# Kernel optimization log

Hardware: AMD Instinct MI355X
Metric: run time of the kernel (lower is better)

The kernel has to match this reference:

```python
import jax, jax.numpy as jnp
import numpy as np

N_USERS, N_NEWS, N_ENT, N_REL, D, K, NNZ = 10000, 10000, 100000, 32, 64, 20, 500000

def setup_inputs() -> dict:
    key = jax.random.key(0)
    ks = jax.random.split(key, 10)
    return {
        "user_emb": jax.random.normal(ks[0], (N_USERS, D), jnp.float32),
        "news_embeding": jax.random.normal(ks[1], (N_NEWS, D), jnp.float32),
        "entity_emb": jax.random.normal(ks[2], (N_ENT, D), jnp.float32),
        "relation_emb": jax.random.normal(ks[3], (N_REL, D), jnp.float32),
        "news_entities": jax.random.randint(ks[4], (N_NEWS, K), 0, N_ENT),
        "news_relations": jnp.zeros((N_NEWS, K), jnp.int32),  # code forces relation id 0 for news
        "neigh_entities": jax.random.randint(ks[5], (N_ENT, K), 0, N_ENT),
        "neigh_relations": jax.random.randint(ks[6], (N_ENT, K), 0, N_REL),
        "interact_rows": jax.random.randint(ks[7], (NNZ,), 0, N_USERS),
        "interact_cols": jax.random.randint(ks[8], (NNZ,), 0, N_NEWS),
        "interact_vals": jax.random.uniform(ks[9], (NNZ,), jnp.float32),
    }

def _sim_hrt(head, tail, rel):
    # head: [N,D], tail/rel: [N,K,D]
    tail_rel = tail * rel                              # [N,K,D]
    head_rel = head[:, None, :] * rel                  # [N,K,D]
    # NOTE: original norms over the NEIGHBOR dim (dim=1), yielding [N,1,D]
    hnorm = jnp.sqrt(jnp.sum(head_rel * head_rel, axis=1))  # [N,D]
    att = jnp.einsum('nkd,nd->nk', tail_rel, hnorm)    # [N,K]
    return att * att

def _agg(head_emb, neigh_ent_emb, neigh_rel_emb):
    w = jax.nn.softmax(_sim_hrt(head_emb, neigh_ent_emb, neigh_rel_emb), axis=-1)
    return jnp.einsum('nk,nkd->nd', w, neigh_ent_emb)

def reference(user_emb, news_embeding, entity_emb, relation_emb,
              news_entities, news_relations, neigh_entities, neigh_relations,
              interact_rows, interact_cols, interact_vals):
    # news aggregation (newsid = arange -> identity gather on news_embeding)
    news_ne = entity_emb[news_entities]                # [N_news,K,D]
    news_nr = relation_emb[news_relations]             # [N_news,K,D]
    news_agg = _agg(news_embeding, news_ne, news_nr)   # [N_news,D]
    # entity aggregation (entities = arange -> identity gather on entity_emb)
    ent_ne = entity_emb[neigh_entities]                # [N_ent,K,D]
    ent_nr = relation_emb[neigh_relations]             # [N_ent,K,D]
    entity_agg = _agg(entity_emb, ent_ne, ent_nr)      # [N_ent,D]
    # user aggregation: sparse interact_mat @ news_agg via segment_sum
    gathered = interact_vals[:, None] * news_agg[interact_cols]  # [NNZ,D]
    user_agg = jax.ops.segment_sum(gathered, interact_rows, num_segments=N_USERS)
    score = jax.nn.softmax(user_emb @ news_agg.T, axis=-1)       # [N_users,N_news]
    user_agg = user_agg + (score @ news_agg) * user_agg
    return (news_agg, entity_agg, user_agg)
```

## Files before the change

### kernel.cpp

```cpp
#include <hip/hip_runtime.h>
#include <hip/hip_bf16.h>


#define DD 64
#define KK 20
#define NCHUNK 313
#define NSL 20
#define NSTRIP 157
#define NUPAD 10048
#define ATSTRIDE 10016
#define PST32 20

#define ATTN_BLOCKS 785
#define AGG_ENT_BLOCKS 12500

typedef __attribute__((ext_vector_type(8))) short short8;
typedef __attribute__((ext_vector_type(4))) float f32x4;

__device__ __forceinline__ unsigned short f2bf(float x) {
    union { __hip_bfloat16 h; unsigned short u; } cv;
    cv.h = __float2bfloat16(x);
    return cv.u;
}
__device__ __forceinline__ float bfu2f(unsigned short u) {
    return __uint_as_float(((unsigned)u) << 16);
}
#define MFMA16(a, b, c) __builtin_amdgcn_mfma_f32_16x16x32_bf16((a), (b), (c), 0, 0, 0)

__device__ __forceinline__
void agg_body(const float* __restrict__ head_emb, const float* __restrict__ ent_emb,
              const float* __restrict__ rel_emb,
              const int* __restrict__ ent_idx, const int* __restrict__ rel_idx,
              float* __restrict__ outp, int bid)
{
    int w = threadIdx.x >> 6;
    int lane = threadIdx.x & 63;
    int half = lane >> 5;
    int l = lane & 31;
    int n0 = bid * 8 + w * 2;

    float2 head = *(const float2*)(head_emb + (long)(n0 + half) * DD + 2 * l);

    float2 tail[KK], trp[KK];
    float2 s2 = make_float2(0.f, 0.f);
#pragma unroll
    for (int k = 0; k < KK; ++k) {
        int ei0 = ent_idx[n0 * KK + k];
        int ei1 = ent_idx[(n0 + 1) * KK + k];
        int ri0 = rel_idx[n0 * KK + k];
        int ri1 = rel_idx[(n0 + 1) * KK + k];
        int e = half ? ei1 : ei0;
        int r = half ? ri1 : ri0;
        float2 rv = *(const float2*)(rel_emb + (long)r * DD + 2 * l);
        float2 tv = *(const float2*)(ent_emb + (long)e * DD + 2 * l);
        tail[k] = tv;
        trp[k] = make_float2(tv.x * rv.x, tv.y * rv.y);
        s2.x = fmaf(rv.x, rv.x, s2.x);
        s2.y = fmaf(rv.y, rv.y, s2.y);
    }
    float2 hn;
    hn.x = fabsf(head.x) * sqrtf(s2.x);
    hn.y = fabsf(head.y) * sqrtf(s2.y);

    float att[KK];
#pragma unroll
    for (int k = 0; k < KK; ++k) {
        float v = fmaf(trp[k].y, hn.y, trp[k].x * hn.x);
#pragma unroll
        for (int m = 1; m < 32; m <<= 1)
            v += __shfl_xor(v, m, 64);
        att[k] = v * v;
    }
    float mx = att[0];
#pragma unroll
    for (int k = 1; k < KK; ++k) mx = fmaxf(mx, att[k]);
    float den = 0.f;
#pragma unroll
    for (int k = 0; k < KK; ++k) { att[k] = __expf(att[k] - mx); den += att[k]; }
    float inv = 1.f / den;
    float2 o = make_float2(0.f, 0.f);
#pragma unroll
    for (int k = 0; k < KK; ++k) {
        o.x = fmaf(att[k], tail[k].x, o.x);
        o.y = fmaf(att[k], tail[k].y, o.y);
    }
    o.x *= inv; o.y *= inv;
    *(float2*)(outp + (long)(n0 + half) * DD + 2 * l) = o;
}

__global__ __launch_bounds__(256)
void agg_kernel(const float* __restrict__ head_emb, const float* __restrict__ ent_emb,
                const float* __restrict__ rel_emb,
                const int* __restrict__ ent_idx, const int* __restrict__ rel_idx,
                float* __restrict__ outp, int N)
{
    int n0 = blockIdx.x * 8 + (threadIdx.x >> 6) * 2;
    if (n0 >= N) return;
    agg_body(head_emb, ent_emb, rel_emb, ent_idx, rel_idx, outp, blockIdx.x);
}

__global__ __launch_bounds__(256)
void cvt_kernel(const float* __restrict__ src, unsigned short* __restrict__ dst,
                int n_src, int n_total)
{
    int t = blockIdx.x * 256 + threadIdx.x;
    if (t >= n_total) return;
    float v = (t < n_src) ? src[t] : 0.f;
    dst[t] = f2bf(v);
}

__global__ __launch_bounds__(256)
void transpose_kernel(const float* __restrict__ src, unsigned short* __restrict__ AT)
{
    __shared__ float T[128][65];
    int t = threadIdx.x;
    int nb = blockIdx.x * 128;
    const float4* s4 = (const float4*)src;
#pragma unroll
    for (int i = 0; i < 8; ++i) {
        int f = i * 256 + t;
        int row = f >> 4;
        int c4 = f & 15;
        int gr = nb + row;
        float4 v = make_float4(0.f, 0.f, 0.f, 0.f);
        if (gr < 10000) v = s4[(long)gr * 16 + c4];
        T[row][c4 * 4 + 0] = v.x;
        T[row][c4 * 4 + 1] = v.y;
        T[row][c4 * 4 + 2] = v.z;
        T[row][c4 * 4 + 3] = v.w;
    }
    __syncthreads();
    int d = t >> 2;
    int seg = t & 3;
#pragma unroll
    for (int g = 0; g < 8; ++g) {
        int nl = seg * 32 + g * 4;
        int n = nb + nl;
        if (n + 3 < ATSTRIDE) {
            int base = seg * 32;
            ushort4 oh;
            oh.x = f2bf(T[base + 2 * g][d]);
            oh.y = f2bf(T[base + 16 + 2 * g][d]);
            oh.z = f2bf(T[base + 2 * g + 1][d]);
            oh.w = f2bf(T[base + 16 + 2 * g + 1][d]);
            *(ushort4*)(AT + (long)d * ATSTRIDE + n) = oh;
        }
    }
}

__global__ __launch_bounds__(256)
void hist_kernel(const int* __restrict__ rows, int* __restrict__ cnt, int nnz)
{
    int e = blockIdx.x * 256 + threadIdx.x;
    if (e < nnz) atomicAdd(&cnt[rows[e]], 1);
}

__global__ __launch_bounds__(256)
void scan_kernel(const int* __restrict__ cnt, int* __restrict__ offs, int* __restrict__ cur)
{
    __shared__ int ssum[256];
    int t = threadIdx.x;
    int loc[40];
    int s = 0;
#pragma unroll
    for (int i = 0; i < 40; ++i) { loc[i] = s; s += cnt[t * 40 + i]; }
    ssum[t] = s;
    __syncthreads();
    int val = s;
    for (int off = 1; off < 256; off <<= 1) {
        int v = (t >= off) ? ssum[t - off] : 0;
        __syncthreads();
        val += v;
        ssum[t] = val;
        __syncthreads();
    }
    int excl = val - s;
#pragma unroll
    for (int i = 0; i < 40; ++i) {
        int o = excl + loc[i];
        offs[t * 40 + i] = o;
        cur[t * 40 + i] = o;
    }
}

__global__ __launch_bounds__(256)
void fill_kernel(const int* __restrict__ rows, int* __restrict__ cur,
                 int* __restrict__ eid, int nnz)
{
    int e = blockIdx.x * 256 + threadIdx.x;
    if (e < nnz) {
        int p = atomicAdd(&cur[rows[e]], 1);
        eid[p] = e;
    }
}

__global__ __launch_bounds__(256)
void gather_kernel(const int* __restrict__ offs, const int* __restrict__ eid,
                   const int* __restrict__ cols, const float* __restrict__ vals,
                   const float* __restrict__ A, float* __restrict__ seg, int n_users)
{
    int w = threadIdx.x >> 6;
    int lane = threadIdx.x & 63;
    int u = blockIdx.x * 4 + w;
    if (u >= n_users) return;
    int s0 = offs[u], s1 = offs[u + 1];
    float acc = 0.f;
    for (int i = s0; i < s1; ++i) {
        int e = eid[i];
        float v = vals[e];
        int c = cols[e];
        acc = fmaf(v, A[(long)c * DD + lane], acc);
    }
    seg[(long)u * DD + lane] = acc;
}

__device__ __forceinline__
void attn_body(const unsigned short* __restrict__ Ubf,
               const unsigned short* __restrict__ Bbf,
               const unsigned short* __restrict__ ATbf,
               float* __restrict__ num, float* __restrict__ den,
               unsigned int* __restrict__ PuAll, int bid)
{
    int w = threadIdx.x >> 6;
    int lane = threadIdx.x & 63;
    int quad = lane >> 4;
    int l15 = lane & 15;
    int wid = bid * 4 + w;
    int strip = wid % NSTRIP;
    int slice = wid / NSTRIP;
    int user0 = strip * 64;

    short8 ua0[4], ua1[4];
#pragma unroll
    for (int t = 0; t < 4; ++t) {
        const short* up = (const short*)Ubf + ((long)(user0 + t * 16 + l15)) * 64;
        ua0[t] = *(const short8*)(up + quad * 8);
        ua1[t] = *(const short8*)(up + 32 + quad * 8);
    }

    f32x4 numC[4][4];
    float dena[4][4];
#pragma unroll
    for (int t = 0; t < 4; ++t)
#pragma unroll
        for (int c = 0; c < 4; ++c) {
            numC[t][c] = (f32x4){0.f, 0.f, 0.f, 0.f};
            dena[t][c] = 0.f;
        }

    for (int ch = slice; ch < NCHUNK; ch += NSL) {
        int nb = ch * 32;
        const short* bh = (const short*)Bbf + ((long)(nb + l15)) * 64;
        short8 b00 = *(const short8*)(bh + quad * 8);
        short8 b01 = *(const short8*)(bh + 32 + quad * 8);
        short8 b10 = *(const short8*)(bh + 16 * 64 + quad * 8);
        short8 b11 = *(const short8*)(bh + 16 * 64 + 32 + quad * 8);

        short8 vh[4];
#pragma unroll
        for (int c = 0; c < 4; ++c)
            vh[c] = *(const short8*)((const short*)ATbf +
                    ((long)(16 * c + l15)) * ATSTRIDE + nb + quad * 8);

        bool vlo = (nb + l15) < 10000;
        bool vhi = (nb + 16 + l15) < 10000;
        f32x4 z = {0.f, 0.f, 0.f, 0.f};
#pragma unroll
        for (int p = 0; p < 2; ++p) {
#pragma unroll
            for (int tt = 0; tt < 2; ++tt) {
                int t = p * 2 + tt;
                f32x4 Llo = MFMA16(ua0[t], b00, z);
                Llo = MFMA16(ua1[t], b01, Llo);
                f32x4 Lhi = MFMA16(ua0[t], b10, z);
                Lhi = MFMA16(ua1[t], b11, Lhi);
                unsigned int* Pt = PuAll + (w * 2 + tt) * (16 * PST32);
#pragma unroll
                for (int r = 0; r < 4; ++r) {
                    float plo = vlo ? __expf(fminf(Llo[r], 70.f)) : 0.f;
                    float phi = vhi ? __expf(fminf(Lhi[r], 70.f)) : 0.f;
                    __hip_bfloat162 pk2 = __float22bfloat162_rn(make_float2(plo, phi));
                    unsigned int pk;
                    __builtin_memcpy(&pk, &pk2, 4);
                    Pt[(quad * 4 + r) * PST32 + l15] = pk;
                    dena[t][r] += __uint_as_float(pk << 16)
                                + __uint_as_float(pk & 0xffff0000u);
                }
            }
            short8 ap[2];
#pragma unroll
            for (int tt = 0; tt < 2; ++tt)
                ap[tt] = *(const short8*)((const short*)(PuAll + (w * 2 + tt) * (16 * PST32)) +
                         l15 * (PST32 * 2) + quad * 8);
#pragma unroll
            for (int c = 0; c < 4; ++c)
#pragma unroll
                for (int tt = 0; tt < 2; ++tt)
                    numC[p * 2 + tt][c] = MFMA16(ap[tt], vh[c], numC[p * 2 + tt][c]);
        }
    }

#pragma unroll
    for (int t = 0; t < 4; ++t)
#pragma unroll
        for (int r = 0; r < 4; ++r) {
#pragma unroll
            for (int m = 1; m < 16; m <<= 1)
                dena[t][r] += __shfl_xor(dena[t][r], m, 64);
        }
    if (l15 == 0) {
#pragma unroll
        for (int t = 0; t < 4; ++t)
#pragma unroll
            for (int r = 0; r < 4; ++r)
                atomicAdd(&den[user0 + t * 16 + quad * 4 + r], dena[t][r]);
    }
#pragma unroll
    for (int t = 0; t < 4; ++t)
#pragma unroll
        for (int c = 0; c < 4; ++c)
#pragma unroll
            for (int r = 0; r < 4; ++r)
                atomicAdd(&num[(long)(user0 + t * 16 + quad * 4 + r) * DD + c * 16 + l15],
                          numC[t][c][r]);
}

__global__ __launch_bounds__(256)
void attn_kernel(const unsigned short* __restrict__ Ubf,
                 const unsigned short* __restrict__ Bbf,
                 const unsigned short* __restrict__ ATbf,
                 float* __restrict__ num, float* __restrict__ den)
{
    __shared__ __align__(16) unsigned int Pu[8][16 * PST32];
    if (blockIdx.x * 4 + (threadIdx.x >> 6) >= NSTRIP * NSL) return;
    attn_body(Ubf, Bbf, ATbf, num, den, &Pu[0][0], blockIdx.x);
}

__global__ __launch_bounds__(256)
void fused_kernel(const unsigned short* __restrict__ Ubf,
                  const unsigned short* __restrict__ Bbf,
                  const unsigned short* __restrict__ ATbf,
                  float* __restrict__ num, float* __restrict__ den,
                  const float* __restrict__ ent_emb, const float* __restrict__ rel_emb,
                  const int* __restrict__ ent_idx, const int* __restrict__ rel_idx,
                  float* __restrict__ out_ent)
{
    __shared__ __align__(16) unsigned int Pu[8][16 * PST32];
    if (blockIdx.x < ATTN_BLOCKS) {
        attn_body(Ubf, Bbf, ATbf, num, den, &Pu[0][0], blockIdx.x);
    } else {
        agg_body(ent_emb, ent_emb, rel_emb, ent_idx, rel_idx, out_ent,
                 blockIdx.x - ATTN_BLOCKS);
    }
}

__global__ __launch_bounds__(256)
void final_kernel(const float* __restrict__ seg, const float* __restrict__ num,
                  const float* __restrict__ den, float* __restrict__ out, int n_users)
{
    int t = blockIdx.x * 256 + threadIdx.x;
    if (t >= n_users * DD) return;
    int u = t >> 6;
    float s = seg[t];
    float o2 = num[t] / den[u];
    out[t] = fmaf(s, o2, s);
}

extern "C" void kernel_launch(void* const* d_in, const int* in_sizes, int n_in,
                              void* d_out, int out_size, void* d_ws, size_t ws_size,
                              hipStream_t stream)
{
    const float* user_emb = (const float*)d_in[0];
    const float* news_emb = (const float*)d_in[1];
    const float* ent_emb  = (const float*)d_in[2];
    const float* rel_emb  = (const float*)d_in[3];
    const int* news_entities   = (const int*)d_in[4];
    const int* news_relations  = (const int*)d_in[5];
    const int* neigh_entities  = (const int*)d_in[6];
    const int* neigh_relations = (const int*)d_in[7];
    const int* interact_rows   = (const int*)d_in[8];
    const int* interact_cols   = (const int*)d_in[9];
    const float* interact_vals = (const float*)d_in[10];

    const int NU = 10000, NN = 10000, NE = 100000, NNZ = 500000;

    float* out_news = (float*)d_out;
    float* out_ent  = out_news + (long)NN * DD;
    float* out_user = out_ent + (long)NE * DD;

    const size_t SCRATCH_F32 =
        640000 + 643072 + 10240 + 10240 + 10240 + 10240 + 500000;
    const size_t SCRATCH_BYTES = SCRATCH_F32 * 4 +
        (size_t)(643072 + 641024 + 641024) * 2;

    bool use_ws = (d_ws != nullptr) && (ws_size >= SCRATCH_BYTES);
    float* base = use_ws ? (float*)d_ws : out_ent;

    float* seg  = base;
    float* num  = seg + 640000;
    float* den  = num + 643072;
    int*   cnt  = (int*)(den + 10240);
    int*   offs = cnt + 10240;
    int*   cur  = offs + 10240;
    int*   eid  = cur + 10240;
    unsigned short* Ubf  = (unsigned short*)(eid + 500000);
    unsigned short* Bbf  = Ubf + 643072;
    unsigned short* ATbf = Bbf + 641024;

    hipMemsetAsync(num, 0, (size_t)(643072 + 10240 + 10240) * sizeof(float), stream);

    agg_kernel<<<NN / 8, 256, 0, stream>>>(news_emb, ent_emb, rel_emb,
                                           news_entities, news_relations, out_news, NN);
    cvt_kernel<<<(NUPAD * DD + 255) / 256, 256, 0, stream>>>(user_emb, Ubf, NU * DD, NUPAD * DD);
    cvt_kernel<<<2504, 256, 0, stream>>>(out_news, Bbf, NN * DD, 10016 * DD);
    transpose_kernel<<<(NN + 127) / 128, 256, 0, stream>>>(out_news, ATbf);
    hist_kernel<<<(NNZ + 255) / 256, 256, 0, stream>>>(interact_rows, cnt, NNZ);
    scan_kernel<<<1, 256, 0, stream>>>(cnt, offs, cur);
    fill_kernel<<<(NNZ + 255) / 256, 256, 0, stream>>>(interact_rows, cur, eid, NNZ);
    gather_kernel<<<(NU + 3) / 4, 256, 0, stream>>>(offs, eid, interact_cols,
                                                    interact_vals, out_news, seg, NU);

    if (use_ws) {
        fused_kernel<<<ATTN_BLOCKS + AGG_ENT_BLOCKS, 256, 0, stream>>>(
            Ubf, Bbf, ATbf, num, den,
            ent_emb, rel_emb, neigh_entities, neigh_relations, out_ent);
        final_kernel<<<(NU * DD + 255) / 256, 256, 0, stream>>>(seg, num, den, out_user, NU);
    } else {
        attn_kernel<<<ATTN_BLOCKS, 256, 0, stream>>>(Ubf, Bbf, ATbf, num, den);
        final_kernel<<<(NU * DD + 255) / 256, 256, 0, stream>>>(seg, num, den, out_user, NU);
        agg_kernel<<<NE / 8, 256, 0, stream>>>(ent_emb, ent_emb, rel_emb,
                                               neigh_entities, neigh_relations, out_ent, NE);
    }
}
```

Before: 456.8 us.

## Merge nine launches into four heterogeneous fused kernels to cut launch gaps

The preprocessing and compute stages are regrouped into four block-partitioned kernels. k1 runs news aggregation, the user bf16 conversion and the CSR histogram. k2 runs the bf16 copy and transpose of news_agg plus the scan. k3 runs attention alongside the CSR fill. k4 runs the user gather alongside entity aggregation. This removes several kernel launches and serial dependency bubbles, and overlaps small independent jobs with large ones. The cost is more complex block dispatch and possible load imbalance inside each fused grid.

```diff
diff --git a/kernel.cpp b/kernel.cpp
--- a/kernel.cpp
+++ b/kernel.cpp
@@ -11,8 +11,20 @@
 #define ATSTRIDE 10016
 #define PST32 20
 
+#define NUC 10000
+#define NNC 10000
+#define NEC 100000
+#define NNZC 500000
+
+#define K1_NEWS 1250
+#define K1_CVTU 628
+#define K1_HIST 512
+#define K1_GRID (K1_NEWS + K1_CVTU + K1_HIST)
 #define ATTN_BLOCKS 785
-#define AGG_ENT_BLOCKS 12500
+#define K3_FILL 512
+#define K3_GRID (ATTN_BLOCKS + K3_FILL)
+#define K4_GATHER 2500
+#define K4_ENT 12500
 
 typedef __attribute__((ext_vector_type(8))) short short8;
 typedef __attribute__((ext_vector_type(4))) float f32x4;
@@ -89,129 +101,111 @@
 }
 
 __global__ __launch_bounds__(256)
-void agg_kernel(const float* __restrict__ head_emb, const float* __restrict__ ent_emb,
-                const float* __restrict__ rel_emb,
-                const int* __restrict__ ent_idx, const int* __restrict__ rel_idx,
-                float* __restrict__ outp, int N)
-{
-    int n0 = blockIdx.x * 8 + (threadIdx.x >> 6) * 2;
-    if (n0 >= N) return;
-    agg_body(head_emb, ent_emb, rel_emb, ent_idx, rel_idx, outp, blockIdx.x);
-}
-
-__global__ __launch_bounds__(256)
-void cvt_kernel(const float* __restrict__ src, unsigned short* __restrict__ dst,
-                int n_src, int n_total)
-{
-    int t = blockIdx.x * 256 + threadIdx.x;
-    if (t >= n_total) return;
-    float v = (t < n_src) ? src[t] : 0.f;
-    dst[t] = f2bf(v);
-}
-
-__global__ __launch_bounds__(256)
-void transpose_kernel(const float* __restrict__ src, unsigned short* __restrict__ AT)
+void k1_kernel(const float* __restrict__ news_emb, const float* __restrict__ ent_emb,
+               const float* __restrict__ rel_emb,
+               const int* __restrict__ news_entities, const int* __restrict__ news_relations,
+               float* __restrict__ out_news,
+               const float* __restrict__ user_emb, unsigned short* __restrict__ Ubf,
+               const int* __restrict__ irows, int* __restrict__ cnt)
+{
+    int bid = blockIdx.x;
+    if (bid < K1_NEWS) {
+        agg_body(news_emb, ent_emb, rel_emb,
+                 news_entities, news_relations, out_news, bid);
+    } else if (bid < K1_NEWS + K1_CVTU) {
+        int i = (bid - K1_NEWS) * 256 + threadIdx.x;
+        int base = i * 4;
+        float4 v = make_float4(0.f, 0.f, 0.f, 0.f);
+        if (base + 3 < NUC * DD) v = *(const float4*)(user_emb + base);
+        ushort4 o;
+        o.x = f2bf(v.x); o.y = f2bf(v.y); o.z = f2bf(v.z); o.w = f2bf(v.w);
+        *(ushort4*)(Ubf + base) = o;
+    } else {
+        int lb = bid - (K1_NEWS + K1_CVTU);
+        for (int e = lb * 256 + threadIdx.x; e < NNZC; e += K1_HIST * 256)
+            atomicAdd(&cnt[irows[e]], 1);
+    }
+}
+
+__global__ __launch_bounds__(256)
+void k2_kernel(const float* __restrict__ src, unsigned short* __restrict__ Bbf,
+               unsigned short* __restrict__ AT,
+               const int* __restrict__ cnt, int* __restrict__ offs, int* __restrict__ cur)
 {
     __shared__ float T[128][65];
-    int t = threadIdx.x;
-    int nb = blockIdx.x * 128;
-    const float4* s4 = (const float4*)src;
-#pragma unroll
-    for (int i = 0; i < 8; ++i) {
-        int f = i * 256 + t;
-        int row = f >> 4;
-        int c4 = f & 15;
-        int gr = nb + row;
-        float4 v = make_float4(0.f, 0.f, 0.f, 0.f);
-        if (gr < 10000) v = s4[(long)gr * 16 + c4];
-        T[row][c4 * 4 + 0] = v.x;
-        T[row][c4 * 4 + 1] = v.y;
-        T[row][c4 * 4 + 2] = v.z;
-        T[row][c4 * 4 + 3] = v.w;
-    }
-    __syncthreads();
-    int d = t >> 2;
-    int seg = t & 3;
-#pragma unroll
-    for (int g = 0; g < 8; ++g) {
-        int nl = seg * 32 + g * 4;
-        int n = nb + nl;
-        if (n + 3 < ATSTRIDE) {
-            int base = seg * 32;
-            ushort4 oh;
-            oh.x = f2bf(T[base + 2 * g][d]);
-            oh.y = f2bf(T[base + 16 + 2 * g][d]);
-            oh.z = f2bf(T[base + 2 * g + 1][d]);
-            oh.w = f2bf(T[base + 16 + 2 * g + 1][d]);
-            *(ushort4*)(AT + (long)d * ATSTRIDE + n) = oh;
-        }
-    }
-}
-
-__global__ __launch_bounds__(256)
-void hist_kernel(const int* __restrict__ rows, int* __restrict__ cnt, int nnz)
-{
-    int e = blockIdx.x * 256 + threadIdx.x;
-    if (e < nnz) atomicAdd(&cnt[rows[e]], 1);
-}
-
-__global__ __launch_bounds__(256)
-void scan_kernel(const int* __restrict__ cnt, int* __restrict__ offs, int* __restrict__ cur)
-{
     __shared__ int ssum[256];
     int t = threadIdx.x;
-    int loc[40];
-    int s = 0;
-#pragma unroll
-    for (int i = 0; i < 40; ++i) { loc[i] = s; s += cnt[t * 40 + i]; }
-    ssum[t] = s;
-    __syncthreads();
-    int val = s;
-    for (int off = 1; off < 256; off <<= 1) {
-        int v = (t >= off) ? ssum[t - off] : 0;
+    if (blockIdx.x < 79) {
+        int nb = blockIdx.x * 128;
+        const float4* s4 = (const float4*)src;
+#pragma unroll
+        for (int i = 0; i < 8; ++i) {
+            int f = i * 256 + t;
+            int row = f >> 4;
+            int c4 = f & 15;
+            int gr = nb + row;
+            float4 v = make_float4(0.f, 0.f, 0.f, 0.f);
+            if (gr < NNC) v = s4[(long)gr * 16 + c4];
+            T[row][c4 * 4 + 0] = v.x;
+            T[row][c4 * 4 + 1] = v.y;
+            T[row][c4 * 4 + 2] = v.z;
+            T[row][c4 * 4 + 3] = v.w;
+        }
         __syncthreads();
-        val += v;
-        ssum[t] = val;
+#pragma unroll
+        for (int i = 0; i < 8; ++i) {
+            int f = i * 256 + t;
+            int row = f >> 4;
+            int q4 = f & 15;
+            int gr = nb + row;
+            if (gr < ATSTRIDE) {
+                ushort4 ob;
+                ob.x = f2bf(T[row][q4 * 4 + 0]);
+                ob.y = f2bf(T[row][q4 * 4 + 1]);
+                ob.z = f2bf(T[row][q4 * 4 + 2]);
+                ob.w = f2bf(T[row][q4 * 4 + 3]);
+                *(ushort4*)(Bbf + (long)gr * 64 + q4 * 4) = ob;
+            }
+        }
+        int d = t >> 2;
+        int seg = t & 3;
+#pragma unroll
+        for (int g = 0; g < 8; ++g) {
+            int nl = seg * 32 + g * 4;
+            int n = nb + nl;
+            if (n + 3 < ATSTRIDE) {
+                int base = seg * 32;
+                ushort4 oh;
+                oh.x = f2bf(T[base + 2 * g][d]);
+                oh.y = f2bf(T[base + 16 + 2 * g][d]);
+                oh.z = f2bf(T[base + 2 * g + 1][d]);
+                oh.w = f2bf(T[base + 16 + 2 * g + 1][d]);
+                *(ushort4*)(AT + (long)d * ATSTRIDE + n) = oh;
+            }
+        }
+    } else {
+        int loc[40];
+        int s = 0;
+#pragma unroll
+        for (int i = 0; i < 40; ++i) { loc[i] = s; s += cnt[t * 40 + i]; }
+        ssum[t] = s;
         __syncthreads();
-    }
-    int excl = val - s;
-#pragma unroll
-    for (int i = 0; i < 40; ++i) {
-        int o = excl + loc[i];
-        offs[t * 40 + i] = o;
-        cur[t * 40 + i] = o;
-    }
-}
-
-__global__ __launch_bounds__(256)
-void fill_kernel(const int* __restrict__ rows, int* __restrict__ cur,
-                 int* __restrict__ eid, int nnz)
-{
-    int e = blockIdx.x * 256 + threadIdx.x;
-    if (e < nnz) {
-        int p = atomicAdd(&cur[rows[e]], 1);
-        eid[p] = e;
-    }
-}
-
-__global__ __launch_bounds__(256)
-void gather_kernel(const int* __restrict__ offs, const int* __restrict__ eid,
-                   const int* __restrict__ cols, const float* __restrict__ vals,
-                   const float* __restrict__ A, float* __restrict__ seg, int n_users)
-{
-    int w = threadIdx.x >> 6;
-    int lane = threadIdx.x & 63;
-    int u = blockIdx.x * 4 + w;
-    if (u >= n_users) return;
-    int s0 = offs[u], s1 = offs[u + 1];
-    float acc = 0.f;
-    for (int i = s0; i < s1; ++i) {
-        int e = eid[i];
-        float v = vals[e];
-        int c = cols[e];
-        acc = fmaf(v, A[(long)c * DD + lane], acc);
-    }
-    seg[(long)u * DD + lane] = acc;
+        int val = s;
+        for (int off = 1; off < 256; off <<= 1) {
+            int v = (t >= off) ? ssum[t - off] : 0;
+            __syncthreads();
+            val += v;
+            ssum[t] = val;
+            __syncthreads();
+        }
+        int excl = val - s;
+#pragma unroll
+        for (int i = 0; i < 40; ++i) {
+            int o = excl + loc[i];
+            offs[t * 40 + i] = o;
+            cur[t * 40 + i] = o;
+        }
+    }
 }
 
 __device__ __forceinline__
@@ -262,8 +256,8 @@
             vh[c] = *(const short8*)((const short*)ATbf +
                     ((long)(16 * c + l15)) * ATSTRIDE + nb + quad * 8);
 
-        bool vlo = (nb + l15) < 10000;
-        bool vhi = (nb + 16 + l15) < 10000;
+        bool vlo = (nb + l15) < NNC;
+        bool vhi = (nb + 16 + l15) < NNC;
         f32x4 z = {0.f, 0.f, 0.f, 0.f};
 #pragma unroll
         for (int p = 0; p < 2; ++p) {
@@ -326,32 +320,62 @@
 }
 
 __global__ __launch_bounds__(256)
-void attn_kernel(const unsigned short* __restrict__ Ubf,
-                 const unsigned short* __restrict__ Bbf,
-                 const unsigned short* __restrict__ ATbf,
-                 float* __restrict__ num, float* __restrict__ den)
+void k3_kernel(const unsigned short* __restrict__ Ubf,
+               const unsigned short* __restrict__ Bbf,
+               const unsigned short* __restrict__ ATbf,
+               float* __restrict__ num, float* __restrict__ den,
+               const int* __restrict__ irows, int* __restrict__ cur,
+               int* __restrict__ eid)
 {
     __shared__ __align__(16) unsigned int Pu[8][16 * PST32];
-    if (blockIdx.x * 4 + (threadIdx.x >> 6) >= NSTRIP * NSL) return;
-    attn_body(Ubf, Bbf, ATbf, num, den, &Pu[0][0], blockIdx.x);
-}
-
-__global__ __launch_bounds__(256)
-void fused_kernel(const unsigned short* __restrict__ Ubf,
-                  const unsigned short* __restrict__ Bbf,
-                  const unsigned short* __restrict__ ATbf,
-                  float* __restrict__ num, float* __restrict__ den,
-                  const float* __restrict__ ent_emb, const float* __restrict__ rel_emb,
-                  const int* __restrict__ ent_idx, const int* __restrict__ rel_idx,
-                  float* __restrict__ out_ent)
-{
-    __shared__ __align__(16) unsigned int Pu[8][16 * PST32];
-    if (blockIdx.x < ATTN_BLOCKS) {
-        attn_body(Ubf, Bbf, ATbf, num, den, &Pu[0][0], blockIdx.x);
+    int bid = blockIdx.x;
+    if (bid < ATTN_BLOCKS) {
+        attn_body(Ubf, Bbf, ATbf, num, den, &Pu[0][0], bid);
     } else {
-        agg_body(ent_emb, ent_emb, rel_emb, ent_idx, rel_idx, out_ent,
-                 blockIdx.x - ATTN_BLOCKS);
-    }
+        int lb = bid - ATTN_BLOCKS;
+        for (int e = lb * 256 + threadIdx.x; e < NNZC; e += K3_FILL * 256) {
+            int p = atomicAdd(&cur[irows[e]], 1);
+            eid[p] = e;
+        }
+    }
+}
+
+__global__ __launch_bounds__(256)
+void k4_kernel(const int* __restrict__ offs, const int* __restrict__ eid,
+               const int* __restrict__ cols, const float* __restrict__ vals,
+               const float* __restrict__ A, float* __restrict__ seg,
+               const float* __restrict__ ent_emb, const float* __restrict__ rel_emb,
+               const int* __restrict__ neigh_entities, const int* __restrict__ neigh_relations,
+               float* __restrict__ out_ent, int ent_blocks)
+{
+    int bid = blockIdx.x;
+    if (bid < K4_GATHER) {
+        int w = threadIdx.x >> 6;
+        int lane = threadIdx.x & 63;
+        int u = bid * 4 + w;
+        if (u >= NUC) return;
+        int s0 = offs[u], s1 = offs[u + 1];
+        float acc = 0.f;
+        for (int i = s0; i < s1; ++i) {
+            int e = eid[i];
+            float v = vals[e];
+            int c = cols[e];
+            acc = fmaf(v, A[(long)c * DD + lane], acc);
+        }
+        seg[(long)u * DD + lane] = acc;
+    } else if (bid < K4_GATHER + ent_blocks) {
+        int lb = bid - K4_GATHER;
+        agg_body(ent_emb, ent_emb, rel_emb,
+                 neigh_entities, neigh_relations, out_ent, lb);
+    }
+}
+
+__global__ __launch_bounds__(256)
+void agg_ent_kernel(const float* __restrict__ ent_emb, const float* __restrict__ rel_emb,
+                    const int* __restrict__ ent_idx, const int* __restrict__ rel_idx,
+                    float* __restrict__ outp)
+{
+    agg_body(ent_emb, ent_emb, rel_emb, ent_idx, rel_idx, outp, blockIdx.x);
 }
 
 __global__ __launch_bounds__(256)
@@ -382,18 +406,17 @@
     const int* interact_cols   = (const int*)d_in[9];
     const float* interact_vals = (const float*)d_in[10];
 
-    const int NU = 10000, NN = 10000, NE = 100000, NNZ = 500000;
+    const int NU = 10000, NN = 10000, NE = 100000;
 
     float* out_news = (float*)d_out;
     float* out_ent  = out_news + (long)NN * DD;
     float* out_user = out_ent + (long)NE * DD;
 
-    const size_t SCRATCH_F32 =
-        640000 + 643072 + 10240 + 10240 + 10240 + 10240 + 500000;
-    const size_t SCRATCH_BYTES = SCRATCH_F32 * 4 +
+    const size_t BASIC_BYTES =
+        (size_t)(640000 + 643072 + 10240 + 10240 + 10240 + 10240 + 500000) * 4 +
         (size_t)(643072 + 641024 + 641024) * 2;
 
-    bool use_ws = (d_ws != nullptr) && (ws_size >= SCRATCH_BYTES);
+    bool use_ws = (d_ws != nullptr) && (ws_size >= BASIC_BYTES);
     float* base = use_ws ? (float*)d_ws : out_ent;
 
     float* seg  = base;
@@ -409,26 +432,26 @@
 
     hipMemsetAsync(num, 0, (size_t)(643072 + 10240 + 10240) * sizeof(float), stream);
 
-    agg_kernel<<<NN / 8, 256, 0, stream>>>(news_emb, ent_emb, rel_emb,
-                                           news_entities, news_relations, out_news, NN);
-    cvt_kernel<<<(NUPAD * DD + 255) / 256, 256, 0, stream>>>(user_emb, Ubf, NU * DD, NUPAD * DD);
-    cvt_kernel<<<2504, 256, 0, stream>>>(out_news, Bbf, NN * DD, 10016 * DD);
-    transpose_kernel<<<(NN + 127) / 128, 256, 0, stream>>>(out_news, ATbf);
-    hist_kernel<<<(NNZ + 255) / 256, 256, 0, stream>>>(interact_rows, cnt, NNZ);
-    scan_kernel<<<1, 256, 0, stream>>>(cnt, offs, cur);
-    fill_kernel<<<(NNZ + 255) / 256, 256, 0, stream>>>(interact_rows, cur, eid, NNZ);
-    gather_kernel<<<(NU + 3) / 4, 256, 0, stream>>>(offs, eid, interact_cols,
-                                                    interact_vals, out_news, seg, NU);
+    k1_kernel<<<K1_GRID, 256, 0, stream>>>(news_emb, ent_emb, rel_emb,
+                                           news_entities, news_relations, out_news,
+                                           user_emb, Ubf, interact_rows, cnt);
+    k2_kernel<<<80, 256, 0, stream>>>(out_news, Bbf, ATbf, cnt, offs, cur);
 
     if (use_ws) {
-        fused_kernel<<<ATTN_BLOCKS + AGG_ENT_BLOCKS, 256, 0, stream>>>(
-            Ubf, Bbf, ATbf, num, den,
-            ent_emb, rel_emb, neigh_entities, neigh_relations, out_ent);
+        k3_kernel<<<K3_GRID, 256, 0, stream>>>(Ubf, Bbf, ATbf, num, den,
+                                               interact_rows, cur, eid);
+        k4_kernel<<<K4_GATHER + K4_ENT, 256, 0, stream>>>(
+            offs, eid, interact_cols, interact_vals, out_news, seg,
+            ent_emb, rel_emb, neigh_entities, neigh_relations, out_ent, K4_ENT);
         final_kernel<<<(NU * DD + 255) / 256, 256, 0, stream>>>(seg, num, den, out_user, NU);
     } else {
-        attn_kernel<<<ATTN_BLOCKS, 256, 0, stream>>>(Ubf, Bbf, ATbf, num, den);
+        k3_kernel<<<K3_GRID, 256, 0, stream>>>(Ubf, Bbf, ATbf, num, den,
+                                               interact_rows, cur, eid);
+        k4_kernel<<<K4_GATHER, 256, 0, stream>>>(
+            offs, eid, interact_cols, interact_vals, out_news, seg,
+            ent_emb, rel_emb, neigh_entities, neigh_relations, out_ent, 0);
         final_kernel<<<(NU * DD + 255) / 256, 256, 0, stream>>>(seg, num, den, out_user, NU);
-        agg_kernel<<<NE / 8, 256, 0, stream>>>(ent_emb, ent_emb, rel_emb,
-                                               neigh_entities, neigh_relations, out_ent, NE);
-    }
-}
+        agg_ent_kernel<<<NE / 8, 256, 0, stream>>>(ent_emb, rel_emb,
+                                                   neigh_entities, neigh_relations, out_ent);
+    }
+}
```

New measurement: 446.5 us. -2.3%, faster.
